# Performance work log

Hardware: AMD Instinct MI355X
Metric: run time of the kernel (lower is better)

The kernel has to match this reference:

```python
import jax, jax.numpy as jnp
import numpy as np

D_MODEL = 1024
NUM_HEADS = 16
D_K = D_MODEL // NUM_HEADS


def setup_inputs() -> dict:
    key = jax.random.key(0)
    ks = jax.random.split(key, 9)
    s = 1.0 / np.sqrt(D_MODEL)
    x = jax.random.normal(ks[0], (4, 2048, D_MODEL), dtype=jnp.float32)
    Wq = jax.random.uniform(ks[1], (D_MODEL, D_MODEL), jnp.float32, -s, s)
    bq = jax.random.uniform(ks[2], (D_MODEL,), jnp.float32, -s, s)
    Wk = jax.random.uniform(ks[3], (D_MODEL, D_MODEL), jnp.float32, -s, s)
    bk = jax.random.uniform(ks[4], (D_MODEL,), jnp.float32, -s, s)
    Wv = jax.random.uniform(ks[5], (D_MODEL, D_MODEL), jnp.float32, -s, s)
    bv = jax.random.uniform(ks[6], (D_MODEL,), jnp.float32, -s, s)
    Wo = jax.random.uniform(ks[7], (D_MODEL, D_MODEL), jnp.float32, -s, s)
    bo = jax.random.uniform(ks[8], (D_MODEL,), jnp.float32, -s, s)
    return {"x": x, "Wq": Wq, "bq": bq, "Wk": Wk, "bk": bk,
            "Wv": Wv, "bv": bv, "Wo": Wo, "bo": bo}


def reference(x, Wq, bq, Wk, bk, Wv, bv, Wo, bo):
    B, S, _ = x.shape
    # project and split heads: [B,S,D] -> [B,H,S,dk]
    def heads(W, b):
        return (x @ W + b).reshape(B, S, NUM_HEADS, D_K).transpose(0, 2, 1, 3)
    q = heads(Wq, bq)
    k = heads(Wk, bk)
    v = heads(Wv, bv)
    scores = jnp.einsum('bhqd,bhkd->bhqk', q, k) / jnp.sqrt(jnp.float32(D_K))
    attn = jax.nn.softmax(scores, axis=-1)
    out = jnp.einsum('bhqk,bhkd->bhqd', attn, v)
    out = out.transpose(0, 2, 1, 3).reshape(B, S, D_MODEL)
    return out @ Wo + bo
```

## Files before the change

kernel.cpp:

```cpp
#include <hip/hip_runtime.h>
#include <hip/hip_bf16.h>

#define D_MODEL 1024
#define NUM_HEADS 16
#define D_K 64
#define B_SZ 4
#define SEQ 2048
#define SCALE_Q 0.180336881f

typedef short bf16x8 __attribute__((ext_vector_type(8)));
typedef float f32x4 __attribute__((ext_vector_type(4)));
typedef unsigned short u16;

__device__ __forceinline__ unsigned cvtpk(float a, float b) {
    unsigned r;
    asm("v_cvt_pk_bf16_f32 %0, %1, %2" : "=v"(r) : "v"(a), "v"(b));
    return r;
}
__device__ __forceinline__ u16 f2bf(float f) {
    return (u16)cvtpk(f, f);
}
__device__ __forceinline__ float exp2a(float x) {
    float r;
    asm("v_exp_f32 %0, %1" : "=v"(r) : "v"(x));
    return r;
}
__device__ __forceinline__ float max3f(float a, float b, float c) {
    float r;
    asm("v_max3_f32 %0, %1, %2, %3" : "=v"(r) : "v"(a), "v"(b), "v"(c));
    return r;
}
__device__ __forceinline__ void gload_lds16(const u16* g, u16* l) {
    __builtin_amdgcn_global_load_lds(
        (const __attribute__((address_space(1))) unsigned int*)g,
        (__attribute__((address_space(3))) unsigned int*)l, 16, 0, 0);
}

__global__ __launch_bounds__(256) void prep_all(
    const float* __restrict__ xin, u16* __restrict__ xbf,
    const float* __restrict__ W0, const float* __restrict__ W1,
    const float* __restrict__ W2, const float* __restrict__ W3,
    u16* __restrict__ Wt)
{
    __shared__ float tile[64][65];
    const int t = threadIdx.x;
    if (blockIdx.x < 1024) {
        const int n8 = (B_SZ * SEQ * D_MODEL) / 8;
        for (int i = blockIdx.x * 256 + t; i < n8; i += 1024 * 256) {
            float4 a = ((const float4*)xin)[(size_t)i * 2];
            float4 b = ((const float4*)xin)[(size_t)i * 2 + 1];
            uint4 o;
            o.x = cvtpk(a.x, a.y);
            o.y = cvtpk(a.z, a.w);
            o.z = cvtpk(b.x, b.y);
            o.w = cvtpk(b.z, b.w);
            ((uint4*)xbf)[i] = o;
        }
        return;
    }
    const int id = blockIdx.x - 1024;
    const int z  = id >> 8;
    const int by = (id >> 4) & 15;
    const int bx = id & 15;
    const float* W = z == 0 ? W0 : z == 1 ? W1 : z == 2 ? W2 : W3;
    u16* out = Wt + (size_t)z * D_MODEL * D_MODEL;
    const int k0 = by * 64;
    const int n0 = bx * 64;
    #pragma unroll
    for (int it = 0; it < 4; ++it) {
        int idx = it * 256 + t;
        int r = idx >> 4;
        int c = (idx & 15) * 4;
        float4 v = *(const float4*)(W + (size_t)(k0 + r) * D_MODEL + n0 + c);
        tile[r][c + 0] = v.x; tile[r][c + 1] = v.y;
        tile[r][c + 2] = v.z; tile[r][c + 3] = v.w;
    }
    __syncthreads();
    #pragma unroll
    for (int it = 0; it < 2; ++it) {
        int idx = it * 256 + t;
        int r = idx >> 3;
        int c = (idx & 7) * 8;
        uint4 o;
        o.x = cvtpk(tile[c + 0][r], tile[c + 1][r]);
        o.y = cvtpk(tile[c + 2][r], tile[c + 3][r]);
        o.z = cvtpk(tile[c + 4][r], tile[c + 5][r]);
        o.w = cvtpk(tile[c + 6][r], tile[c + 7][r]);
        *(uint4*)(out + (size_t)(n0 + r) * D_MODEL + k0 + c) = o;
    }
}

__global__ __launch_bounds__(256) void gemm_qkv(
    const u16* __restrict__ A, const u16* __restrict__ Wt,
    const float* __restrict__ bq, const float* __restrict__ bk,
    const float* __restrict__ bv, u16* __restrict__ Yb)
{
    __shared__ u16 As[128][64];
    __shared__ u16 Bs[128][64];
    const int t    = threadIdx.x;
    const int lane = t & 63;
    const int wv   = t >> 6;
    const int wm   = wv >> 1, wn = wv & 1;
    const int g    = lane >> 4;
    const int lr   = lane & 15;
    const int m0   = blockIdx.y * 128;
    const int n0   = blockIdx.x * 128;
    const int K    = D_MODEL;

    const int srow = lane >> 3;
    const int scol = (lane & 7) * 8;

    f32x4 acc[4][4];
    #pragma unroll
    for (int i = 0; i < 4; ++i)
        #pragma unroll
        for (int j = 0; j < 4; ++j)
            acc[i][j] = (f32x4){0.f, 0.f, 0.f, 0.f};

    for (int k0 = 0; k0 < K; k0 += 64) {
        if (k0) __syncthreads();
        #pragma unroll
        for (int it = 0; it < 4; ++it) {
            const int r = wv * 32 + it * 8;
            gload_lds16(A  + (size_t)(m0 + r + srow) * K + k0 + scol, &As[r][0]);
            gload_lds16(Wt + (size_t)(n0 + r + srow) * K + k0 + scol, &Bs[r][0]);
        }
        __syncthreads();

        #pragma unroll
        for (int s = 0; s < 2; ++s) {
            bf16x8 af[4], bfr[4];
            #pragma unroll
            for (int mt = 0; mt < 4; ++mt)
                af[mt] = *(const bf16x8*)(&As[wm * 64 + mt * 16 + lr][g * 8 + s * 32]);
            #pragma unroll
            for (int nt = 0; nt < 4; ++nt)
                bfr[nt] = *(const bf16x8*)(&Bs[wn * 64 + nt * 16 + lr][g * 8 + s * 32]);
            #pragma unroll
            for (int mt = 0; mt < 4; ++mt)
                #pragma unroll
                for (int nt = 0; nt < 4; ++nt)
                    acc[mt][nt] = __builtin_amdgcn_mfma_f32_16x16x32_bf16(
                        af[mt], bfr[nt], acc[mt][nt], 0, 0, 0);
        }
    }

    const int which = n0 >> 10;
    const float scale = (which == 0) ? SCALE_Q : 1.0f;
    const float* bp = (which == 0) ? bq : (which == 1) ? bk : bv;
    u16* dst = Yb + (size_t)which * ((size_t)B_SZ * SEQ * D_MODEL);

    float bv4[4];
    #pragma unroll
    for (int nt = 0; nt < 4; ++nt)
        bv4[nt] = bp[((n0 + wn * 64 + nt * 16 + lr) & 1023)];

    #pragma unroll
    for (int mt = 0; mt < 4; ++mt) {
        #pragma unroll
        for (int nt = 0; nt < 4; ++nt) {
            #pragma unroll
            for (int r = 0; r < 4; ++r) {
                const int m = m0 + wm * 64 + mt * 16 + g * 4 + r;
                const int nn = (n0 + wn * 64 + nt * 16 + lr) & 1023;
                const float val = (acc[mt][nt][r] + bv4[nt]) * scale;
                const int b = m >> 11, s2 = m & 2047;
                const int h = nn >> 6, d = nn & 63;
                if (which == 2) {
                    const int z  = s2 & 63;
                    const int zp = (z & 32) + 8 * ((z & 15) >> 2) + (z & 3) + 4 * ((z >> 4) & 1);
                    const int col = zp ^ ((d & 7) << 3);
                    dst[(((size_t)(b * NUM_HEADS + h) * D_K + d) * SEQ) + (s2 & ~63) + col] = f2bf(val);
                } else {
                    const int dd = (which == 1) ? (d ^ ((s2 & 7) << 3)) : d;
                    dst[(((size_t)(b * NUM_HEADS + h) * SEQ) + s2) * D_K + dd] = f2bf(val);
                }
            }
        }
    }
}

__global__ __launch_bounds__(256) void gemm_o(
    const u16* __restrict__ A, const u16* __restrict__ Wt,
    const float* __restrict__ bias, float* __restrict__ Y)
{
    __shared__ u16 As[128][64];
    __shared__ u16 Bs[128][64];
    const int t    = threadIdx.x;
    const int lane = t & 63;
    const int wv   = t >> 6;
    const int wm   = wv >> 1, wn = wv & 1;
    const int g    = lane >> 4;
    const int lr   = lane & 15;
    const int m0   = blockIdx.y * 128;
    const int n0   = blockIdx.x * 128;
    const int K    = D_MODEL;

    const int srow = lane >> 3;
    const int scol = (lane & 7) * 8;

    f32x4 acc[4][4];
    #pragma unroll
    for (int i = 0; i < 4; ++i)
        #pragma unroll
        for (int j = 0; j < 4; ++j)
            acc[i][j] = (f32x4){0.f, 0.f, 0.f, 0.f};

    for (int k0 = 0; k0 < K; k0 += 64) {
        if (k0) __syncthreads();
        #pragma unroll
        for (int it = 0; it < 4; ++it) {
            const int r = wv * 32 + it * 8;
            gload_lds16(A  + (size_t)(m0 + r + srow) * K + k0 + scol, &As[r][0]);
            gload_lds16(Wt + (size_t)(n0 + r + srow) * K + k0 + scol, &Bs[r][0]);
        }
        __syncthreads();

        #pragma unroll
        for (int s = 0; s < 2; ++s) {
            bf16x8 af[4], bfr[4];
            #pragma unroll
            for (int mt = 0; mt < 4; ++mt)
                af[mt] = *(const bf16x8*)(&As[wm * 64 + mt * 16 + lr][g * 8 + s * 32]);
            #pragma unroll
            for (int nt = 0; nt < 4; ++nt)
                bfr[nt] = *(const bf16x8*)(&Bs[wn * 64 + nt * 16 + lr][g * 8 + s * 32]);
            #pragma unroll
            for (int mt = 0; mt < 4; ++mt)
                #pragma unroll
                for (int nt = 0; nt < 4; ++nt)
                    acc[mt][nt] = __builtin_amdgcn_mfma_f32_16x16x32_bf16(
                        af[mt], bfr[nt], acc[mt][nt], 0, 0, 0);
        }
    }

    float bv4[4];
    #pragma unroll
    for (int nt = 0; nt < 4; ++nt) bv4[nt] = bias[n0 + wn * 64 + nt * 16 + lr];

    #pragma unroll
    for (int mt = 0; mt < 4; ++mt)
        #pragma unroll
        for (int nt = 0; nt < 4; ++nt)
            #pragma unroll
            for (int r = 0; r < 4; ++r) {
                const int m = m0 + wm * 64 + mt * 16 + g * 4 + r;
                const int n = n0 + wn * 64 + nt * 16 + lr;
                Y[(size_t)m * D_MODEL + n] = acc[mt][nt][r] + bv4[nt];
            }
}

__global__ __launch_bounds__(512, 4) void attn_mfma(
    const u16* __restrict__ Q, const u16* __restrict__ Kb,
    const u16* __restrict__ Vt, u16* __restrict__ ctx)
{
    __shared__ u16 Ks[2][128][64];
    __shared__ u16 Vs[2][64][128];
    const int t    = threadIdx.x;
    const int lane = t & 63;
    const int w    = t >> 6;
    const int g    = lane >> 4;
    const int lr   = lane & 15;
    const int qt   = blockIdx.x;
    const int h    = blockIdx.y;
    const int b    = blockIdx.z;
    const size_t hoff = ((size_t)b * NUM_HEADS + h) * SEQ * D_K;

    bf16x8 qf[2][2];
    #pragma unroll
    for (int u = 0; u < 2; ++u) {
        const int q = qt * 256 + w * 32 + u * 16 + lr;
        qf[u][0] = *(const bf16x8*)(Q + hoff + (size_t)q * D_K + g * 8);
        qf[u][1] = *(const bf16x8*)(Q + hoff + (size_t)q * D_K + g * 8 + 32);
    }

    const int krow = w * 16 + (lane >> 3);
    const int kcol = (lane & 7) * 8;
    const u16* ksrc = Kb + hoff + (size_t)krow * D_K + kcol;
    const int vrow = w * 8 + (lane >> 4);
    const int vcol = (lane & 15) * 8;
    const u16* vsrc = Vt + hoff + (size_t)vrow * SEQ + vcol;

    const int xm = (lr & 7) << 3;

    float mrun[2]  = {0.f, 0.f};
    float lpart[2] = {0.f, 0.f};
    f32x4 acc_o[2][4];
    #pragma unroll
    for (int u = 0; u < 2; ++u)
        #pragma unroll
        for (int n = 0; n < 4; ++n) acc_o[u][n] = (f32x4){0.f, 0.f, 0.f, 0.f};

    gload_lds16(ksrc,               &Ks[0][w * 16][0]);
    gload_lds16(ksrc + 8 * D_K,     &Ks[0][w * 16 + 8][0]);
    gload_lds16(vsrc,               &Vs[0][w * 8][0]);
    gload_lds16(vsrc + 4 * SEQ,     &Vs[0][w * 8 + 4][0]);

    int bu = 0;
    for (int kt = 0; kt < SEQ / 128; ++kt) {
        __syncthreads();
        if (kt + 1 < SEQ / 128) {
            const size_t kv0 = (size_t)(kt + 1) * 128;
            const int nb = bu ^ 1;
            gload_lds16(ksrc + kv0 * D_K,       &Ks[nb][w * 16][0]);
            gload_lds16(ksrc + (kv0 + 8) * D_K, &Ks[nb][w * 16 + 8][0]);
            gload_lds16(vsrc + kv0,             &Vs[nb][w * 8][0]);
            gload_lds16(vsrc + 4 * SEQ + kv0,   &Vs[nb][w * 8 + 4][0]);
        }

        #pragma unroll
        for (int hv = 0; hv < 2; ++hv) {
            f32x4 sc[2][4];
            #pragma unroll
            for (int u = 0; u < 2; ++u) {
                const f32x4 mi = {-mrun[u], -mrun[u], -mrun[u], -mrun[u]};
                #pragma unroll
                for (int mt = 0; mt < 4; ++mt) sc[u][mt] = mi;
            }
            __builtin_amdgcn_s_setprio(1);
            #pragma unroll
            for (int s = 0; s < 2; ++s)
                #pragma unroll
                for (int mt = 0; mt < 4; ++mt) {
                    bf16x8 kf = *(const bf16x8*)(
                        &Ks[bu][hv * 64 + mt * 16 + lr][(g * 8 + s * 32) ^ xm]);
                    sc[0][mt] = __builtin_amdgcn_mfma_f32_16x16x32_bf16(kf, qf[0][s], sc[0][mt], 0, 0, 0);
                    sc[1][mt] = __builtin_amdgcn_mfma_f32_16x16x32_bf16(kf, qf[1][s], sc[1][mt], 0, 0, 0);
                }
            __builtin_amdgcn_s_setprio(0);

            union { bf16x8 v; unsigned u[4]; } pa[2][2];
            #pragma unroll
            for (int u = 0; u < 2; ++u) {
                float t0 = max3f(sc[u][0][0], sc[u][0][1], sc[u][0][2]);
                float t1 = max3f(sc[u][0][3], sc[u][1][0], sc[u][1][1]);
                float t2 = max3f(sc[u][1][2], sc[u][1][3], sc[u][2][0]);
                float t3 = max3f(sc[u][2][1], sc[u][2][2], sc[u][2][3]);
                float t4 = max3f(sc[u][3][0], sc[u][3][1], sc[u][3][2]);
                float tmax = fmaxf(max3f(t0, t1, t2), max3f(t3, t4, sc[u][3][3]));

                if (!__all(tmax <= 8.0f)) {
                    float rowmax = fmaxf(tmax, __shfl_xor(tmax, 16));
                    rowmax = fmaxf(rowmax, __shfl_xor(rowmax, 32));
                    const float excess = fmaxf(rowmax, 0.0f);
                    const float alpha = exp2a(-excess);
                    mrun[u] += excess;
                    lpart[u] *= alpha;
                    float ar[4];
                    #pragma unroll
                    for (int r = 0; r < 4; ++r) ar[r] = __shfl(alpha, g * 4 + r);
                    #pragma unroll
                    for (int n = 0; n < 4; ++n) {
                        f32x4 v = acc_o[u][n];
                        #pragma unroll
                        for (int r = 0; r < 4; ++r) v[r] *= ar[r];
                        acc_o[u][n] = v;
                    }
                    #pragma unroll
                    for (int mt = 0; mt < 4; ++mt)
                        #pragma unroll
                        for (int r = 0; r < 4; ++r) sc[u][mt][r] -= excess;
                }

                float lsum = 0.f;
                #pragma unroll
                for (int mt = 0; mt < 4; ++mt)
                    #pragma unroll
                    for (int r = 0; r < 4; ++r) {
                        const float e = exp2a(sc[u][mt][r]);
                        sc[u][mt][r] = e;
                        lsum += e;
                    }
                lpart[u] += lsum;

                #pragma unroll
                for (int s = 0; s < 2; ++s) {
                    pa[u][s].u[0] = cvtpk(sc[u][2 * s][0],     sc[u][2 * s][1]);
                    pa[u][s].u[1] = cvtpk(sc[u][2 * s][2],     sc[u][2 * s][3]);
                    pa[u][s].u[2] = cvtpk(sc[u][2 * s + 1][0], sc[u][2 * s + 1][1]);
                    pa[u][s].u[3] = cvtpk(sc[u][2 * s + 1][2], sc[u][2 * s + 1][3]);
                }
            }

            __builtin_amdgcn_s_setprio(1);
            #pragma unroll
            for (int s = 0; s < 2; ++s)
                #pragma unroll
                for (int n = 0; n < 4; ++n) {
                    bf16x8 vf = *(const bf16x8*)(
                        &Vs[bu][16 * n + lr][hv * 64 + ((32 * s + 8 * g) ^ xm)]);
                    acc_o[0][n] = __builtin_amdgcn_mfma_f32_16x16x32_bf16(pa[0][s].v, vf, acc_o[0][n], 0, 0, 0);
                    acc_o[1][n] = __builtin_amdgcn_mfma_f32_16x16x32_bf16(pa[1][s].v, vf, acc_o[1][n], 0, 0, 0);
                }
            __builtin_amdgcn_s_setprio(0);
        }
        bu ^= 1;
    }

    #pragma unroll
    for (int u = 0; u < 2; ++u) {
        float l = lpart[u];
        l += __shfl_xor(l, 16);
        l += __shfl_xor(l, 32);
        const float linv = 1.0f / l;
        float lr4[4];
        #pragma unroll
        for (int r = 0; r < 4; ++r) lr4[r] = __shfl(linv, g * 4 + r);
        #pragma unroll
        for (int n = 0; n < 4; ++n)
            #pragma unroll
            for (int r = 0; r < 4; ++r) {
                const int qrow = qt * 256 + w * 32 + u * 16 + 4 * g + r;
                ctx[((size_t)b * SEQ + qrow) * D_MODEL + h * D_K + 16 * n + lr] =
                    f2bf(acc_o[u][n][r] * lr4[r]);
            }
    }
}

extern "C" void kernel_launch(void* const* d_in, const int* in_sizes, int n_in,
                              void* d_out, int out_size, void* d_ws, size_t ws_size,
                              hipStream_t stream)
{
    const float* x  = (const float*)d_in[0];
    const float* Wq = (const float*)d_in[1];
    const float* bq = (const float*)d_in[2];
    const float* Wk = (const float*)d_in[3];
    const float* bk = (const float*)d_in[4];
    const float* Wv = (const float*)d_in[5];
    const float* bv = (const float*)d_in[6];
    const float* Wo = (const float*)d_in[7];
    const float* bo = (const float*)d_in[8];
    float* out = (float*)d_out;

    char* ws = (char*)d_ws;
    const size_t MB = 1024 * 1024;
    u16* xbf  = (u16*)(ws);
    u16* Wt   = (u16*)(ws + 16 * MB);
    u16* Qbf  = (u16*)(ws + 24 * MB);
    u16* ctxb = (u16*)(ws + 72 * MB);
    u16* Kbf  = Qbf + (size_t)B_SZ * SEQ * D_MODEL;
    u16* Vtw  = Kbf + (size_t)B_SZ * SEQ * D_MODEL;

    prep_all<<<2048, 256, 0, stream>>>(x, xbf, Wq, Wk, Wv, Wo, Wt);

    gemm_qkv<<<dim3(3 * D_MODEL / 128, (B_SZ * SEQ) / 128), 256, 0, stream>>>(
        xbf, Wt, bq, bk, bv, Qbf);

    attn_mfma<<<dim3(SEQ / 256, NUM_HEADS, B_SZ), 512, 0, stream>>>(Qbf, Kbf, Vtw, ctxb);

    gemm_o<<<dim3(D_MODEL / 128, (B_SZ * SEQ) / 128), 256, 0, stream>>>(
        ctxb, Wt + 3 * (size_t)D_MODEL * D_MODEL, bo, out);
}
```

Baseline: 194.8 us.

## Double-buffer GEMM LDS tiles, remap blocks across XCDs, vectorize V-transpose stores

Both projection GEMMs now use two LDS buffers and prefetch the next K tile while computing on the current one, dropping one barrier per iteration and overlapping global loads with MFMA work. Block indices in the GEMMs and the attention kernel are remapped so that consecutive hardware block IDs, which are spread round-robin over the 8 XCDs, work on neighbouring tiles, with the aim of better L2 reuse per XCD. The V-transposed epilogue now writes four bf16 values as one 8-byte store, relying on the permuted column layout keeping those four values contiguous. Doubling the LDS buffers raises shared-memory use per block and may lower occupancy.

```diff
diff --git a/kernel.cpp b/kernel.cpp
--- a/kernel.cpp
+++ b/kernel.cpp
@@ -95,16 +95,18 @@
     const float* __restrict__ bq, const float* __restrict__ bk,
     const float* __restrict__ bv, u16* __restrict__ Yb)
 {
-    __shared__ u16 As[128][64];
-    __shared__ u16 Bs[128][64];
+    __shared__ u16 As[2][128][64];
+    __shared__ u16 Bs[2][128][64];
     const int t    = threadIdx.x;
     const int lane = t & 63;
     const int wv   = t >> 6;
     const int wm   = wv >> 1, wn = wv & 1;
     const int g    = lane >> 4;
     const int lr   = lane & 15;
-    const int m0   = blockIdx.y * 128;
-    const int n0   = blockIdx.x * 128;
+    const int fid  = blockIdx.y * 24 + blockIdx.x;
+    const int oid  = (fid & 7) * 192 + (fid >> 3);
+    const int m0   = (oid / 24) * 128;
+    const int n0   = (oid % 24) * 128;
     const int K    = D_MODEL;
 
     const int srow = lane >> 3;
@@ -117,25 +119,34 @@
         for (int j = 0; j < 4; ++j)
             acc[i][j] = (f32x4){0.f, 0.f, 0.f, 0.f};
 
+    #pragma unroll
+    for (int it = 0; it < 4; ++it) {
+        const int r = wv * 32 + it * 8;
+        gload_lds16(A  + (size_t)(m0 + r + srow) * K + scol, &As[0][r][0]);
+        gload_lds16(Wt + (size_t)(n0 + r + srow) * K + scol, &Bs[0][r][0]);
+    }
+
     for (int k0 = 0; k0 < K; k0 += 64) {
-        if (k0) __syncthreads();
-        #pragma unroll
-        for (int it = 0; it < 4; ++it) {
-            const int r = wv * 32 + it * 8;
-            gload_lds16(A  + (size_t)(m0 + r + srow) * K + k0 + scol, &As[r][0]);
-            gload_lds16(Wt + (size_t)(n0 + r + srow) * K + k0 + scol, &Bs[r][0]);
-        }
+        const int cur = (k0 >> 6) & 1;
         __syncthreads();
-
+        if (k0 + 64 < K) {
+            const int nb = cur ^ 1;
+            #pragma unroll
+            for (int it = 0; it < 4; ++it) {
+                const int r = wv * 32 + it * 8;
+                gload_lds16(A  + (size_t)(m0 + r + srow) * K + k0 + 64 + scol, &As[nb][r][0]);
+                gload_lds16(Wt + (size_t)(n0 + r + srow) * K + k0 + 64 + scol, &Bs[nb][r][0]);
+            }
+        }
         #pragma unroll
         for (int s = 0; s < 2; ++s) {
             bf16x8 af[4], bfr[4];
             #pragma unroll
             for (int mt = 0; mt < 4; ++mt)
-                af[mt] = *(const bf16x8*)(&As[wm * 64 + mt * 16 + lr][g * 8 + s * 32]);
+                af[mt] = *(const bf16x8*)(&As[cur][wm * 64 + mt * 16 + lr][g * 8 + s * 32]);
             #pragma unroll
             for (int nt = 0; nt < 4; ++nt)
-                bfr[nt] = *(const bf16x8*)(&Bs[wn * 64 + nt * 16 + lr][g * 8 + s * 32]);
+                bfr[nt] = *(const bf16x8*)(&Bs[cur][wn * 64 + nt * 16 + lr][g * 8 + s * 32]);
             #pragma unroll
             for (int mt = 0; mt < 4; ++mt)
                 #pragma unroll
@@ -159,21 +170,27 @@
     for (int mt = 0; mt < 4; ++mt) {
         #pragma unroll
         for (int nt = 0; nt < 4; ++nt) {
-            #pragma unroll
-            for (int r = 0; r < 4; ++r) {
-                const int m = m0 + wm * 64 + mt * 16 + g * 4 + r;
-                const int nn = (n0 + wn * 64 + nt * 16 + lr) & 1023;
-                const float val = (acc[mt][nt][r] + bv4[nt]) * scale;
-                const int b = m >> 11, s2 = m & 2047;
-                const int h = nn >> 6, d = nn & 63;
-                if (which == 2) {
-                    const int z  = s2 & 63;
-                    const int zp = (z & 32) + 8 * ((z & 15) >> 2) + (z & 3) + 4 * ((z >> 4) & 1);
-                    const int col = zp ^ ((d & 7) << 3);
-                    dst[(((size_t)(b * NUM_HEADS + h) * D_K + d) * SEQ) + (s2 & ~63) + col] = f2bf(val);
-                } else {
-                    const int dd = (which == 1) ? (d ^ ((s2 & 7) << 3)) : d;
-                    dst[(((size_t)(b * NUM_HEADS + h) * SEQ) + s2) * D_K + dd] = f2bf(val);
+            float v4[4];
+            #pragma unroll
+            for (int r = 0; r < 4; ++r) v4[r] = (acc[mt][nt][r] + bv4[nt]) * scale;
+            const int mbase = m0 + wm * 64 + mt * 16 + g * 4;
+            const int nn = (n0 + wn * 64 + nt * 16 + lr) & 1023;
+            const int h = nn >> 6, d = nn & 63;
+            const int bb = mbase >> 11, s2 = mbase & 2047;
+            if (which == 2) {
+                const int z  = s2 & 63;
+                const int zp = (z & 32) + 8 * ((z & 15) >> 2) + 4 * ((z >> 4) & 1);
+                const int col = zp ^ ((d & 7) << 3);
+                uint2 o;
+                o.x = cvtpk(v4[0], v4[1]);
+                o.y = cvtpk(v4[2], v4[3]);
+                *(uint2*)&dst[(((size_t)(bb * NUM_HEADS + h) * D_K + d) * SEQ) + (s2 & ~63) + col] = o;
+            } else {
+                #pragma unroll
+                for (int r = 0; r < 4; ++r) {
+                    const int s2r = s2 + r;
+                    const int dd = (which == 1) ? (d ^ ((s2r & 7) << 3)) : d;
+                    dst[(((size_t)(bb * NUM_HEADS + h) * SEQ) + s2r) * D_K + dd] = f2bf(v4[r]);
                 }
             }
         }
@@ -184,16 +201,18 @@
     const u16* __restrict__ A, const u16* __restrict__ Wt,
     const float* __restrict__ bias, float* __restrict__ Y)
 {
-    __shared__ u16 As[128][64];
-    __shared__ u16 Bs[128][64];
+    __shared__ u16 As[2][128][64];
+    __shared__ u16 Bs[2][128][64];
     const int t    = threadIdx.x;
     const int lane = t & 63;
     const int wv   = t >> 6;
     const int wm   = wv >> 1, wn = wv & 1;
     const int g    = lane >> 4;
     const int lr   = lane & 15;
-    const int m0   = blockIdx.y * 128;
-    const int n0   = blockIdx.x * 128;
+    const int fid  = blockIdx.y * 8 + blockIdx.x;
+    const int oid  = (fid & 7) * 64 + (fid >> 3);
+    const int m0   = (oid >> 3) * 128;
+    const int n0   = (oid & 7) * 128;
     const int K    = D_MODEL;
 
     const int srow = lane >> 3;
@@ -206,25 +225,34 @@
         for (int j = 0; j < 4; ++j)
             acc[i][j] = (f32x4){0.f, 0.f, 0.f, 0.f};
 
+    #pragma unroll
+    for (int it = 0; it < 4; ++it) {
+        const int r = wv * 32 + it * 8;
+        gload_lds16(A  + (size_t)(m0 + r + srow) * K + scol, &As[0][r][0]);
+        gload_lds16(Wt + (size_t)(n0 + r + srow) * K + scol, &Bs[0][r][0]);
+    }
+
     for (int k0 = 0; k0 < K; k0 += 64) {
-        if (k0) __syncthreads();
-        #pragma unroll
-        for (int it = 0; it < 4; ++it) {
-            const int r = wv * 32 + it * 8;
-            gload_lds16(A  + (size_t)(m0 + r + srow) * K + k0 + scol, &As[r][0]);
-            gload_lds16(Wt + (size_t)(n0 + r + srow) * K + k0 + scol, &Bs[r][0]);
-        }
+        const int cur = (k0 >> 6) & 1;
         __syncthreads();
-
+        if (k0 + 64 < K) {
+            const int nb = cur ^ 1;
+            #pragma unroll
+            for (int it = 0; it < 4; ++it) {
+                const int r = wv * 32 + it * 8;
+                gload_lds16(A  + (size_t)(m0 + r + srow) * K + k0 + 64 + scol, &As[nb][r][0]);
+                gload_lds16(Wt + (size_t)(n0 + r + srow) * K + k0 + 64 + scol, &Bs[nb][r][0]);
+            }
+        }
         #pragma unroll
         for (int s = 0; s < 2; ++s) {
             bf16x8 af[4], bfr[4];
             #pragma unroll
             for (int mt = 0; mt < 4; ++mt)
-                af[mt] = *(const bf16x8*)(&As[wm * 64 + mt * 16 + lr][g * 8 + s * 32]);
+                af[mt] = *(const bf16x8*)(&As[cur][wm * 64 + mt * 16 + lr][g * 8 + s * 32]);
             #pragma unroll
             for (int nt = 0; nt < 4; ++nt)
-                bfr[nt] = *(const bf16x8*)(&Bs[wn * 64 + nt * 16 + lr][g * 8 + s * 32]);
+                bfr[nt] = *(const bf16x8*)(&Bs[cur][wn * 64 + nt * 16 + lr][g * 8 + s * 32]);
             #pragma unroll
             for (int mt = 0; mt < 4; ++mt)
                 #pragma unroll
@@ -261,9 +289,11 @@
     const int w    = t >> 6;
     const int g    = lane >> 4;
     const int lr   = lane & 15;
-    const int qt   = blockIdx.x;
-    const int h    = blockIdx.y;
-    const int b    = blockIdx.z;
+    const int fid  = blockIdx.x + (blockIdx.y << 3) + (blockIdx.z << 7);
+    const int oid  = (fid & 7) * 64 + (fid >> 3);
+    const int qt   = oid & 7;
+    const int h    = (oid >> 3) & 15;
+    const int b    = oid >> 7;
     const size_t hoff = ((size_t)b * NUM_HEADS + h) * SEQ * D_K;
 
     bf16x8 qf[2][2];
```

Measured after the change: 194.6 us. Within noise of the previous version (-0.1%).
